# Kernel tuning notes

Hardware: AMD Instinct MI355X
Metric: run time of the kernel (lower is better)

Reference implementation:

```python
import jax, jax.numpy as jnp
import numpy as np

ALPHA = 0.2          # LeakyReLU negative slope
NEG_INF = -9e15      # mask value used by the original pygat implementation


def gat_layer(x, adj, W, a_src, a_dst, concat):
    """Dense multi-head GAT layer (pygat-style GraphAttentionLayer).

    x: [N, F_in], adj: [N, N] bool, W: [K, F_in, H], a_src/a_dst: [K, H].
    Returns [N, K*H] (concat=True, with ELU) or [N, H] (concat=False, mean heads).
    """
    h = jnp.einsum('nf,kfh->knh', x, W)                      # [K, N, H]
    f_src = jnp.einsum('knh,kh->kn', h, a_src)               # [K, N]
    f_dst = jnp.einsum('knh,kh->kn', h, a_dst)               # [K, N]
    e = jax.nn.leaky_relu(f_src[:, :, None] + f_dst[:, None, :], ALPHA)  # [K, N, N]
    e = jnp.where(adj[None, :, :], e, NEG_INF)
    att = jax.nn.softmax(e, axis=-1)                         # masked softmax over neighbors
    out = jnp.einsum('knm,kmh->knh', att, h)                 # [K, N, H]
    if concat:
        K, N, H = out.shape
        return jax.nn.elu(jnp.transpose(out, (1, 0, 2)).reshape(N, K * H))
    return out.mean(axis=0)                                  # [N, H]


def setup_inputs() -> dict:
    key = jax.random.key(0)
    ks = jax.random.split(key, 8)
    N, Fdim, H, K, C = 8192, 512, 128, 2, 16
    x = jax.random.normal(ks[0], (N, Fdim), dtype=jnp.float32)
    # sparse-ish binary adjacency, avg degree ~32, with self loops
    adj = jax.random.uniform(ks[1], (N, N)) < (32.0 / N)
    adj = adj | jnp.eye(N, dtype=bool)
    s1 = 1.0 / np.sqrt(Fdim)
    s2 = 1.0 / np.sqrt(K * H)
    W1 = jax.random.normal(ks[2], (K, Fdim, H), dtype=jnp.float32) * s1
    a1_src = jax.random.normal(ks[3], (K, H), dtype=jnp.float32) * s1
    a1_dst = jax.random.normal(ks[4], (K, H), dtype=jnp.float32) * s1
    W2 = jax.random.normal(ks[5], (1, K * H, C), dtype=jnp.float32) * s2
    a2_src = jax.random.normal(ks[6], (1, C), dtype=jnp.float32) * s2
    a2_dst = jax.random.normal(ks[7], (1, C), dtype=jnp.float32) * s2
    return {"x": x, "adj": adj, "W1": W1, "a1_src": a1_src, "a1_dst": a1_dst,
            "W2": W2, "a2_src": a2_src, "a2_dst": a2_dst}


def reference(x, adj, W1, a1_src, a1_dst, W2, a2_src, a2_dst):
    h1 = gat_layer(x, adj, W1, a1_src, a1_dst, concat=True)   # [N, K*H]
    h1 = jax.nn.relu(h1)                                      # dropout p=0.0 -> identity
    out = gat_layer(h1, adj, W2, a2_src, a2_dst, concat=False)  # [N, C]
    return out
```

## Files before the change

### kernel.cpp

```cpp
#include <hip/hip_runtime.h>
#include <hip/hip_bf16.h>
#include <math.h>

constexpr int NN   = 8192;
constexpr int FIN  = 512;
constexpr int HC   = 256;
constexpr int COUT = 16;
constexpr int MAXD = 128;

__device__ __forceinline__ float lrelu(float x) { return x > 0.f ? x : 0.2f * x; }

__global__ __launch_bounds__(64) void detect_kernel(const int* __restrict__ adj32,
                                                    int* __restrict__ flag) {
  int lane = threadIdx.x;
  size_t idx = (size_t)(lane * 32) * (size_t)(NN + 1);
  int v = adj32[idx];
  bool four = (v == 1) || (v == 0x3f800000);
  unsigned long long b = __ballot(four);
  if (lane == 0) flag[0] = (b == ~0ull) ? 1 : 0;
}

__global__ __launch_bounds__(256) void build_csr(const void* __restrict__ adj,
                                                 const int* __restrict__ flag,
                                                 int* __restrict__ nbr,
                                                 int* __restrict__ cnt) {
  __shared__ int scnt;
  int i = blockIdx.x;
  if (threadIdx.x == 0) scnt = 0;
  __syncthreads();
  int* row_out = nbr + (size_t)i * MAXD;
  if (flag[0]) {
    const int4* row = reinterpret_cast<const int4*>((const int*)adj + (size_t)i * NN);
#pragma unroll
    for (int rep = 0; rep < 8; ++rep) {
      int vi = rep * 256 + threadIdx.x;
      int4 v = row[vi];
      int base = vi * 4;
      if (v.x) { int p = atomicAdd(&scnt, 1); if (p < MAXD) row_out[p] = base; }
      if (v.y) { int p = atomicAdd(&scnt, 1); if (p < MAXD) row_out[p] = base + 1; }
      if (v.z) { int p = atomicAdd(&scnt, 1); if (p < MAXD) row_out[p] = base + 2; }
      if (v.w) { int p = atomicAdd(&scnt, 1); if (p < MAXD) row_out[p] = base + 3; }
    }
  } else {
    const uint4* row = reinterpret_cast<const uint4*>((const unsigned char*)adj + (size_t)i * NN);
#pragma unroll
    for (int rep = 0; rep < 2; ++rep) {
      int vi = rep * 256 + threadIdx.x;
      uint4 v = row[vi];
      int base = vi * 16;
      unsigned w[4] = {v.x, v.y, v.z, v.w};
#pragma unroll
      for (int q = 0; q < 4; ++q)
#pragma unroll
        for (int b = 0; b < 4; ++b)
          if ((w[q] >> (8 * b)) & 0xffu) {
            int p = atomicAdd(&scnt, 1);
            if (p < MAXD) row_out[p] = base + q * 4 + b;
          }
    }
  }
  __syncthreads();
  if (threadIdx.x == 0) cnt[i] = scnt < MAXD ? scnt : MAXD;
}

__global__ __launch_bounds__(256) void repack_w1(const float* __restrict__ W1,
                                                 float* __restrict__ Wc) {
  int idx = blockIdx.x * 256 + threadIdx.x;
  int h = idx & 127;
  int f = (idx >> 7) & 511;
  int k = idx >> 16;
  Wc[f * HC + k * 128 + h] = W1[idx];
}

__global__ __launch_bounds__(256) void gemm1_kernel(const float* __restrict__ X,
                                                    const float* __restrict__ B,
                                                    float* __restrict__ Hout) {
  __shared__ float As[16][64];
  __shared__ float Bs[16][64];
  int tid = threadIdx.x;
  int brow = blockIdx.x * 64;
  int bcol = blockIdx.y * 64;
  int tr = (tid >> 4) * 4;
  int tc = (tid & 15) * 4;
  float acc[4][4] = {};
  int lr = tid >> 2;
  int lk = (tid & 3) * 4;
  int bk = tid >> 4;
  int bc = (tid & 15) * 4;
  for (int k0 = 0; k0 < FIN; k0 += 16) {
    float4 av = *reinterpret_cast<const float4*>(X + (size_t)(brow + lr) * FIN + k0 + lk);
    As[lk + 0][lr] = av.x; As[lk + 1][lr] = av.y;
    As[lk + 2][lr] = av.z; As[lk + 3][lr] = av.w;
    float4 bv = *reinterpret_cast<const float4*>(B + (size_t)(k0 + bk) * HC + bcol + bc);
    *reinterpret_cast<float4*>(&Bs[bk][bc]) = bv;
    __syncthreads();
#pragma unroll
    for (int kk = 0; kk < 16; ++kk) {
      float a0 = As[kk][tr + 0], a1 = As[kk][tr + 1];
      float a2 = As[kk][tr + 2], a3 = As[kk][tr + 3];
      float4 b4 = *reinterpret_cast<const float4*>(&Bs[kk][tc]);
      acc[0][0] += a0 * b4.x; acc[0][1] += a0 * b4.y; acc[0][2] += a0 * b4.z; acc[0][3] += a0 * b4.w;
      acc[1][0] += a1 * b4.x; acc[1][1] += a1 * b4.y; acc[1][2] += a1 * b4.z; acc[1][3] += a1 * b4.w;
      acc[2][0] += a2 * b4.x; acc[2][1] += a2 * b4.y; acc[2][2] += a2 * b4.z; acc[2][3] += a2 * b4.w;
      acc[3][0] += a3 * b4.x; acc[3][1] += a3 * b4.y; acc[3][2] += a3 * b4.z; acc[3][3] += a3 * b4.w;
    }
    __syncthreads();
  }
#pragma unroll
  for (int r = 0; r < 4; ++r) {
    float4 o = make_float4(acc[r][0], acc[r][1], acc[r][2], acc[r][3]);
    *reinterpret_cast<float4*>(Hout + (size_t)(brow + tr + r) * HC + bcol + tc) = o;
  }
}

__global__ __launch_bounds__(256) void f1_kernel(const float* __restrict__ H,
                                                 const float* __restrict__ a_src,
                                                 const float* __restrict__ a_dst,
                                                 float* __restrict__ fs,
                                                 float* __restrict__ fd) {
  int wave = threadIdx.x >> 6, lane = threadIdx.x & 63;
  int n = blockIdx.x * 4 + wave;
  const float* hr = H + (size_t)n * HC;
  float h0 = hr[lane], h1 = hr[lane + 64], h2 = hr[lane + 128], h3 = hr[lane + 192];
  float s0 = h0 * a_src[lane] + h1 * a_src[lane + 64];
  float s1 = h2 * a_src[lane + 128] + h3 * a_src[lane + 192];
  float d0 = h0 * a_dst[lane] + h1 * a_dst[lane + 64];
  float d1 = h2 * a_dst[lane + 128] + h3 * a_dst[lane + 192];
#pragma unroll
  for (int off = 32; off > 0; off >>= 1) {
    s0 += __shfl_xor(s0, off);
    s1 += __shfl_xor(s1, off);
    d0 += __shfl_xor(d0, off);
    d1 += __shfl_xor(d1, off);
  }
  if (lane == 0) {
    fs[n] = s0; fs[NN + n] = s1;
    fd[n] = d0; fd[NN + n] = d1;
  }
}

__global__ __launch_bounds__(256) void attn1_kernel(const int* __restrict__ nbr,
                                                    const int* __restrict__ cnt,
                                                    const float* __restrict__ H,
                                                    const float* __restrict__ fs,
                                                    const float* __restrict__ fd,
                                                    float* __restrict__ H1) {
  __shared__ float att[2][MAXD];
  __shared__ int jidx[MAXD];
  int i = blockIdx.x;
  int t = threadIdx.x;
  int deg = cnt[i];
  if (t < MAXD && t < deg) {
    int j = nbr[(size_t)i * MAXD + t];
    jidx[t] = j;
    att[0][t] = lrelu(fs[i] + fd[j]);
    att[1][t] = lrelu(fs[NN + i] + fd[NN + j]);
  }
  __syncthreads();
  int wave = t >> 6, lane = t & 63;
  if (wave < 2) {
    int k = wave;
    float e0 = (lane < deg) ? att[k][lane] : -INFINITY;
    float e1 = (lane + 64 < deg) ? att[k][lane + 64] : -INFINITY;
    float m = fmaxf(e0, e1);
#pragma unroll
    for (int off = 32; off > 0; off >>= 1) m = fmaxf(m, __shfl_xor(m, off));
    float p0 = (lane < deg) ? expf(e0 - m) : 0.f;
    float p1 = (lane + 64 < deg) ? expf(e1 - m) : 0.f;
    float s = p0 + p1;
#pragma unroll
    for (int off = 32; off > 0; off >>= 1) s += __shfl_xor(s, off);
    float inv = 1.f / s;
    if (lane < deg) att[k][lane] = p0 * inv;
    if (lane + 64 < deg) att[k][lane + 64] = p1 * inv;
  }
  __syncthreads();
  int k = t >> 7;
  float acc = 0.f;
  for (int q = 0; q < deg; ++q) acc += att[k][q] * H[(size_t)jidx[q] * HC + t];
  H1[(size_t)i * HC + t] = fmaxf(acc, 0.f);
}

__global__ __launch_bounds__(256) void gemm2_kernel(const float* __restrict__ H1,
                                                    const float* __restrict__ W2,
                                                    const float* __restrict__ a2s,
                                                    const float* __restrict__ a2d,
                                                    float* __restrict__ H2,
                                                    float* __restrict__ f2s,
                                                    float* __restrict__ f2d) {
  __shared__ float Ws[HC * COUT];
  int tid = threadIdx.x;
#pragma unroll
  for (int r = 0; r < 16; ++r) Ws[r * 256 + tid] = W2[r * 256 + tid];
  __syncthreads();
  int rg = tid >> 4, c = tid & 15;
  int n = blockIdx.x * 16 + rg;
  const float* h1r = H1 + (size_t)n * HC;
  float acc = 0.f;
#pragma unroll 8
  for (int kk = 0; kk < HC; ++kk) acc += h1r[kk] * Ws[kk * COUT + c];
  H2[(size_t)n * COUT + c] = acc;
  float s = acc * a2s[c];
  float d = acc * a2d[c];
#pragma unroll
  for (int off = 8; off > 0; off >>= 1) {
    s += __shfl_xor(s, off, 16);
    d += __shfl_xor(d, off, 16);
  }
  if (c == 0) { f2s[n] = s; f2d[n] = d; }
}

__global__ __launch_bounds__(64) void attn2_kernel(const int* __restrict__ nbr,
                                                   const int* __restrict__ cnt,
                                                   const float* __restrict__ H2,
                                                   const float* __restrict__ fs,
                                                   const float* __restrict__ fd,
                                                   float* __restrict__ out) {
  __shared__ float att[MAXD];
  __shared__ int jj[MAXD];
  int i = blockIdx.x;
  int lane = threadIdx.x;
  int deg = cnt[i];
  float fsi = fs[i];
  int j0 = (lane < deg) ? nbr[(size_t)i * MAXD + lane] : 0;
  int j1 = (lane + 64 < deg) ? nbr[(size_t)i * MAXD + lane + 64] : 0;
  float e0 = (lane < deg) ? lrelu(fsi + fd[j0]) : -INFINITY;
  float e1 = (lane + 64 < deg) ? lrelu(fsi + fd[j1]) : -INFINITY;
  float m = fmaxf(e0, e1);
#pragma unroll
  for (int off = 32; off > 0; off >>= 1) m = fmaxf(m, __shfl_xor(m, off));
  float p0 = (lane < deg) ? expf(e0 - m) : 0.f;
  float p1 = (lane + 64 < deg) ? expf(e1 - m) : 0.f;
  float s = p0 + p1;
#pragma unroll
  for (int off = 32; off > 0; off >>= 1) s += __shfl_xor(s, off);
  float inv = 1.f / s;
  att[lane] = p0 * inv;
  att[lane + 64] = p1 * inv;
  jj[lane] = j0;
  jj[lane + 64] = j1;
  __syncthreads();
  if (lane < COUT) {
    float acc = 0.f;
    for (int q = 0; q < deg; ++q) acc += att[q] * H2[(size_t)jj[q] * COUT + lane];
    out[(size_t)i * COUT + lane] = acc;
  }
}

extern "C" void kernel_launch(void* const* d_in, const int* in_sizes, int n_in,
                              void* d_out, int out_size, void* d_ws, size_t ws_size,
                              hipStream_t stream) {
  const float* x   = (const float*)d_in[0];
  const void*  adj = d_in[1];
  const float* W1  = (const float*)d_in[2];
  const float* a1s = (const float*)d_in[3];
  const float* a1d = (const float*)d_in[4];
  const float* W2  = (const float*)d_in[5];
  const float* a2s = (const float*)d_in[6];
  const float* a2d = (const float*)d_in[7];
  float* out = (float*)d_out;

  char* ws = (char*)d_ws;
  size_t off = 0;
  auto alloc = [&](size_t bytes) -> void* {
    void* p = ws + off;
    off = (off + bytes + 255) & ~(size_t)255;
    return p;
  };
  int*   flag = (int*)  alloc(4);
  int*   nbr  = (int*)  alloc((size_t)NN * MAXD * 4);
  int*   cnt  = (int*)  alloc((size_t)NN * 4);
  float* Wc   = (float*)alloc((size_t)FIN * HC * 4);
  float* H    = (float*)alloc((size_t)NN * HC * 4);
  float* fs   = (float*)alloc((size_t)2 * NN * 4);
  float* fd   = (float*)alloc((size_t)2 * NN * 4);
  float* H1   = (float*)alloc((size_t)NN * HC * 4);
  float* H2   = (float*)alloc((size_t)NN * COUT * 4);
  float* f2s  = (float*)alloc((size_t)NN * 4);
  float* f2d  = (float*)alloc((size_t)NN * 4);

  hipLaunchKernelGGL(detect_kernel, dim3(1), dim3(64), 0, stream, (const int*)adj, flag);
  hipLaunchKernelGGL(build_csr, dim3(NN), dim3(256), 0, stream, adj, flag, nbr, cnt);
  hipLaunchKernelGGL(repack_w1, dim3(512), dim3(256), 0, stream, W1, Wc);
  hipLaunchKernelGGL(gemm1_kernel, dim3(128, 4), dim3(256), 0, stream, x, Wc, H);
  hipLaunchKernelGGL(f1_kernel, dim3(NN / 4), dim3(256), 0, stream, H, a1s, a1d, fs, fd);
  hipLaunchKernelGGL(attn1_kernel, dim3(NN), dim3(256), 0, stream, nbr, cnt, H, fs, fd, H1);
  hipLaunchKernelGGL(gemm2_kernel, dim3(NN / 16), dim3(256), 0, stream, H1, W2, a2s, a2d, H2, f2s, f2d);
  hipLaunchKernelGGL(attn2_kernel, dim3(NN), dim3(64), 0, stream, nbr, cnt, H2, f2s, f2d, out);
}
```

Measured before the change: 460.8 us.

## Replace FP32 SIMT GEMM with split-bf16 MFMA GEMM and unroll attention gather

The first-layer projection GEMM moves from a shared-memory FP32 FMA kernel to MFMA bf16 instructions. Inputs and weights are split into high and low bf16 parts, and three products are accumulated to keep close to FP32 accuracy. Two conversion kernels now pre-split X and a transposed W1, which adds extra memory traffic for X. The attention aggregation loop is also unrolled by four so several neighbour gathers are in flight at once.

```diff
diff --git a/kernel.cpp b/kernel.cpp
--- a/kernel.cpp
+++ b/kernel.cpp
@@ -8,7 +8,19 @@
 constexpr int COUT = 16;
 constexpr int MAXD = 128;
 
+typedef __attribute__((ext_vector_type(8))) short bf16x8;
+typedef __attribute__((ext_vector_type(4))) float f32x4;
+
 __device__ __forceinline__ float lrelu(float x) { return x > 0.f ? x : 0.2f * x; }
+
+__device__ __forceinline__ unsigned short f2bf(float f) {
+  unsigned u = __float_as_uint(f);
+  return (unsigned short)((u + 0x7fffu + ((u >> 16) & 1u)) >> 16);
+}
+__device__ __forceinline__ float bf2f(unsigned short h) {
+  unsigned u = ((unsigned)h) << 16;
+  return __uint_as_float(u);
+}
 
 __global__ __launch_bounds__(64) void detect_kernel(const int* __restrict__ adj32,
                                                     int* __restrict__ flag) {
@@ -63,54 +75,75 @@
   if (threadIdx.x == 0) cnt[i] = scnt < MAXD ? scnt : MAXD;
 }
 
-__global__ __launch_bounds__(256) void repack_w1(const float* __restrict__ W1,
-                                                 float* __restrict__ Wc) {
+__global__ __launch_bounds__(256) void convert_x(const float* __restrict__ x,
+                                                 unsigned short* __restrict__ Xh,
+                                                 unsigned short* __restrict__ Xl) {
+  int t = blockIdx.x * 256 + threadIdx.x;
+  float4 v = *reinterpret_cast<const float4*>(x + (size_t)t * 4);
+  ushort4 hi, lo;
+  hi.x = f2bf(v.x); lo.x = f2bf(v.x - bf2f(hi.x));
+  hi.y = f2bf(v.y); lo.y = f2bf(v.y - bf2f(hi.y));
+  hi.z = f2bf(v.z); lo.z = f2bf(v.z - bf2f(hi.z));
+  hi.w = f2bf(v.w); lo.w = f2bf(v.w - bf2f(hi.w));
+  *reinterpret_cast<ushort4*>(Xh + (size_t)t * 4) = hi;
+  *reinterpret_cast<ushort4*>(Xl + (size_t)t * 4) = lo;
+}
+
+__global__ __launch_bounds__(256) void convert_w(const float* __restrict__ W1,
+                                                 unsigned short* __restrict__ Wth,
+                                                 unsigned short* __restrict__ Wtl) {
   int idx = blockIdx.x * 256 + threadIdx.x;
-  int h = idx & 127;
-  int f = (idx >> 7) & 511;
-  int k = idx >> 16;
-  Wc[f * HC + k * 128 + h] = W1[idx];
-}
-
-__global__ __launch_bounds__(256) void gemm1_kernel(const float* __restrict__ X,
-                                                    const float* __restrict__ B,
-                                                    float* __restrict__ Hout) {
-  __shared__ float As[16][64];
-  __shared__ float Bs[16][64];
-  int tid = threadIdx.x;
-  int brow = blockIdx.x * 64;
-  int bcol = blockIdx.y * 64;
-  int tr = (tid >> 4) * 4;
-  int tc = (tid & 15) * 4;
-  float acc[4][4] = {};
-  int lr = tid >> 2;
-  int lk = (tid & 3) * 4;
-  int bk = tid >> 4;
-  int bc = (tid & 15) * 4;
-  for (int k0 = 0; k0 < FIN; k0 += 16) {
-    float4 av = *reinterpret_cast<const float4*>(X + (size_t)(brow + lr) * FIN + k0 + lk);
-    As[lk + 0][lr] = av.x; As[lk + 1][lr] = av.y;
-    As[lk + 2][lr] = av.z; As[lk + 3][lr] = av.w;
-    float4 bv = *reinterpret_cast<const float4*>(B + (size_t)(k0 + bk) * HC + bcol + bc);
-    *reinterpret_cast<float4*>(&Bs[bk][bc]) = bv;
-    __syncthreads();
-#pragma unroll
-    for (int kk = 0; kk < 16; ++kk) {
-      float a0 = As[kk][tr + 0], a1 = As[kk][tr + 1];
-      float a2 = As[kk][tr + 2], a3 = As[kk][tr + 3];
-      float4 b4 = *reinterpret_cast<const float4*>(&Bs[kk][tc]);
-      acc[0][0] += a0 * b4.x; acc[0][1] += a0 * b4.y; acc[0][2] += a0 * b4.z; acc[0][3] += a0 * b4.w;
-      acc[1][0] += a1 * b4.x; acc[1][1] += a1 * b4.y; acc[1][2] += a1 * b4.z; acc[1][3] += a1 * b4.w;
-      acc[2][0] += a2 * b4.x; acc[2][1] += a2 * b4.y; acc[2][2] += a2 * b4.z; acc[2][3] += a2 * b4.w;
-      acc[3][0] += a3 * b4.x; acc[3][1] += a3 * b4.y; acc[3][2] += a3 * b4.z; acc[3][3] += a3 * b4.w;
+  int n = idx >> 9, kk = idx & 511;
+  int k = n >> 7, h = n & 127;
+  float v = W1[k * 65536 + kk * 128 + h];
+  unsigned short hi = f2bf(v);
+  Wth[idx] = hi;
+  Wtl[idx] = f2bf(v - bf2f(hi));
+}
+
+__global__ __launch_bounds__(256) void gemm1m(const unsigned short* __restrict__ Xh,
+                                              const unsigned short* __restrict__ Xl,
+                                              const unsigned short* __restrict__ Bh,
+                                              const unsigned short* __restrict__ Bl,
+                                              float* __restrict__ Hout) {
+  int wave = threadIdx.x >> 6, lane = threadIdx.x & 63;
+  int rowBase = blockIdx.x * 128 + wave * 32;
+  int colBase = blockIdx.y * 64;
+  int frow = lane & 15;
+  int kchunk = (lane >> 4) * 8;
+  f32x4 acc[2][4] = {};
+  for (int k0 = 0; k0 < FIN; k0 += 32) {
+    bf16x8 ah[2], al[2], bh[4], bl[4];
+#pragma unroll
+    for (int r = 0; r < 2; ++r) {
+      size_t off = (size_t)(rowBase + r * 16 + frow) * FIN + k0 + kchunk;
+      ah[r] = *reinterpret_cast<const bf16x8*>(Xh + off);
+      al[r] = *reinterpret_cast<const bf16x8*>(Xl + off);
     }
-    __syncthreads();
-  }
-#pragma unroll
-  for (int r = 0; r < 4; ++r) {
-    float4 o = make_float4(acc[r][0], acc[r][1], acc[r][2], acc[r][3]);
-    *reinterpret_cast<float4*>(Hout + (size_t)(brow + tr + r) * HC + bcol + tc) = o;
-  }
+#pragma unroll
+    for (int c = 0; c < 4; ++c) {
+      size_t off = (size_t)(colBase + c * 16 + frow) * FIN + k0 + kchunk;
+      bh[c] = *reinterpret_cast<const bf16x8*>(Bh + off);
+      bl[c] = *reinterpret_cast<const bf16x8*>(Bl + off);
+    }
+#pragma unroll
+    for (int r = 0; r < 2; ++r)
+#pragma unroll
+      for (int c = 0; c < 4; ++c) {
+        acc[r][c] = __builtin_amdgcn_mfma_f32_16x16x32_bf16(ah[r], bh[c], acc[r][c], 0, 0, 0);
+        acc[r][c] = __builtin_amdgcn_mfma_f32_16x16x32_bf16(ah[r], bl[c], acc[r][c], 0, 0, 0);
+        acc[r][c] = __builtin_amdgcn_mfma_f32_16x16x32_bf16(al[r], bh[c], acc[r][c], 0, 0, 0);
+      }
+  }
+  int dcol = lane & 15, drow4 = (lane >> 4) * 4;
+#pragma unroll
+  for (int r = 0; r < 2; ++r)
+#pragma unroll
+    for (int c = 0; c < 4; ++c)
+#pragma unroll
+      for (int q = 0; q < 4; ++q)
+        Hout[(size_t)(rowBase + r * 16 + drow4 + q) * HC + colBase + c * 16 + dcol] =
+            acc[r][c][q];
 }
 
 __global__ __launch_bounds__(256) void f1_kernel(const float* __restrict__ H,
@@ -177,7 +210,17 @@
   __syncthreads();
   int k = t >> 7;
   float acc = 0.f;
-  for (int q = 0; q < deg; ++q) acc += att[k][q] * H[(size_t)jidx[q] * HC + t];
+  int q = 0;
+  for (; q + 4 <= deg; q += 4) {
+    float a0 = att[k][q], a1 = att[k][q + 1], a2 = att[k][q + 2], a3 = att[k][q + 3];
+    int j0 = jidx[q], j1 = jidx[q + 1], j2 = jidx[q + 2], j3 = jidx[q + 3];
+    float g0 = H[(size_t)j0 * HC + t];
+    float g1 = H[(size_t)j1 * HC + t];
+    float g2 = H[(size_t)j2 * HC + t];
+    float g3 = H[(size_t)j3 * HC + t];
+    acc += a0 * g0 + a1 * g1 + a2 * g2 + a3 * g3;
+  }
+  for (; q < deg; ++q) acc += att[k][q] * H[(size_t)jidx[q] * HC + t];
   H1[(size_t)i * HC + t] = fmaxf(acc, 0.f);
 }
 
@@ -267,22 +310,26 @@
     off = (off + bytes + 255) & ~(size_t)255;
     return p;
   };
-  int*   flag = (int*)  alloc(4);
-  int*   nbr  = (int*)  alloc((size_t)NN * MAXD * 4);
-  int*   cnt  = (int*)  alloc((size_t)NN * 4);
-  float* Wc   = (float*)alloc((size_t)FIN * HC * 4);
-  float* H    = (float*)alloc((size_t)NN * HC * 4);
-  float* fs   = (float*)alloc((size_t)2 * NN * 4);
-  float* fd   = (float*)alloc((size_t)2 * NN * 4);
-  float* H1   = (float*)alloc((size_t)NN * HC * 4);
-  float* H2   = (float*)alloc((size_t)NN * COUT * 4);
-  float* f2s  = (float*)alloc((size_t)NN * 4);
-  float* f2d  = (float*)alloc((size_t)NN * 4);
+  int*            flag = (int*)           alloc(4);
+  int*            nbr  = (int*)           alloc((size_t)NN * MAXD * 4);
+  int*            cnt  = (int*)           alloc((size_t)NN * 4);
+  unsigned short* Xh   = (unsigned short*)alloc((size_t)NN * FIN * 2);
+  unsigned short* Xl   = (unsigned short*)alloc((size_t)NN * FIN * 2);
+  unsigned short* Wth  = (unsigned short*)alloc((size_t)HC * FIN * 2);
+  unsigned short* Wtl  = (unsigned short*)alloc((size_t)HC * FIN * 2);
+  float*          H    = (float*)         alloc((size_t)NN * HC * 4);
+  float*          fs   = (float*)         alloc((size_t)2 * NN * 4);
+  float*          fd   = (float*)         alloc((size_t)2 * NN * 4);
+  float*          H1   = (float*)         alloc((size_t)NN * HC * 4);
+  float*          H2   = (float*)         alloc((size_t)NN * COUT * 4);
+  float*          f2s  = (float*)         alloc((size_t)NN * 4);
+  float*          f2d  = (float*)         alloc((size_t)NN * 4);
 
   hipLaunchKernelGGL(detect_kernel, dim3(1), dim3(64), 0, stream, (const int*)adj, flag);
   hipLaunchKernelGGL(build_csr, dim3(NN), dim3(256), 0, stream, adj, flag, nbr, cnt);
-  hipLaunchKernelGGL(repack_w1, dim3(512), dim3(256), 0, stream, W1, Wc);
-  hipLaunchKernelGGL(gemm1_kernel, dim3(128, 4), dim3(256), 0, stream, x, Wc, H);
+  hipLaunchKernelGGL(convert_x, dim3(NN * FIN / 1024), dim3(256), 0, stream, x, Xh, Xl);
+  hipLaunchKernelGGL(convert_w, dim3(HC * FIN / 256), dim3(256), 0, stream, W1, Wth, Wtl);
+  hipLaunchKernelGGL(gemm1m, dim3(NN / 128, HC / 64), dim3(256), 0, stream, Xh, Xl, Wth, Wtl, H);
   hipLaunchKernelGGL(f1_kernel, dim3(NN / 4), dim3(256), 0, stream, H, a1s, a1d, fs, fd);
   hipLaunchKernelGGL(attn1_kernel, dim3(NN), dim3(256), 0, stream, nbr, cnt, H, fs, fd, H1);
   hipLaunchKernelGGL(gemm2_kernel, dim3(NN / 16), dim3(256), 0, stream, H1, W2, a2s, a2d, H2, f2s, f2d);
```

Measured after the change: 459.4 us. Within noise of the previous version (-0.3%).
